# Kernel optimization log

Hardware: AMD Instinct MI355X
Metric: run time of the kernel (lower is better)

The kernel has to match this reference:

```python
import jax, jax.numpy as jnp
import numpy as np

EPS = 1e-8  # torch CosineSimilarity default eps

def _normalize(x):
    # torch clamps each norm at eps before dividing
    n = jnp.sqrt(jnp.sum(x * x, axis=-1, keepdims=True))
    return x / jnp.maximum(n, EPS)

def _cross_entropy(logits, labels):
    logp = jax.nn.log_softmax(logits, axis=-1)
    return -jnp.mean(jnp.take_along_axis(logp, labels[:, None], axis=-1))

def setup_inputs() -> dict:
    key = jax.random.key(0)
    ks = jax.random.split(key, 7)
    B, M, D = 8192, 3129, 512
    return {
        'mm_proj': jax.random.normal(ks[0], (B, D), jnp.float32),
        'ans_embedding': jax.random.normal(ks[1], (M, D), jnp.float32),
        'v_max': jax.random.normal(ks[2], (B, D), jnp.float32),
        'mm': jax.random.normal(ks[3], (B, D), jnp.float32),
        'logits_q': jax.random.normal(ks[4], (B, M), jnp.float32),
        'logits_rubi': jax.random.normal(ks[5], (B, M), jnp.float32),
        'class_id': jax.random.randint(ks[6], (B, 1), 0, M, jnp.int64),
    }

def reference(mm_proj, ans_embedding, v_max, mm, logits_q, logits_rubi, class_id,
              question_loss_weight=1.0):
    cid = class_id.squeeze(1)  # [B]
    # NCE over cosine similarities: fuse normalize + GEMM instead of [B,M,D] expand
    g = _normalize(mm_proj)          # [B, D]
    a = _normalize(ans_embedding)    # [M, D]
    d_logit = jnp.einsum('bd,md->bm', g, a)  # [B, M] cosine matrix
    positive_dist = jnp.take_along_axis(d_logit, cid[:, None], axis=1)[:, 0]  # [B]
    num = jnp.exp(positive_dist)
    den = jnp.sum(jnp.exp(d_logit), axis=-1)
    loss_nce = jnp.mean(-jnp.log(num / den))
    # object cosine loss
    obj_dist = jnp.sum(_normalize(v_max) * _normalize(mm), axis=-1)  # [B]
    obj_loss = jnp.mean(1.0 - obj_dist)
    fusion_loss = (_cross_entropy(logits_rubi, cid) + obj_loss + loss_nce) / 3.0
    question_loss = _cross_entropy(logits_q, cid)
    loss = fusion_loss + question_loss_weight * question_loss
    # out['loss'], out['loss_mm_q'], out['loss_q']
    return jnp.stack([loss, fusion_loss, question_loss])
```

## Files before the change

### kernel.cpp

```cpp
#include <hip/hip_runtime.h>
#include <hip/hip_bf16.h>

#define B_N 8192
#define M_N 3129
#define M_PAD 3200
#define D_N 512

#define CE_L 12
#define CE_SPAN (CE_L * 256)
#define CE_WPA 8344
#define CE_WTOT (2 * CE_WPA)
#define CE1_SPANS 10688
#define CE2_SPANS (CE_WTOT - CE1_SPANS)
#define CE1_BLOCKS (CE1_SPANS / 4)
#define CE2_BLOCKS (CE2_SPANS / 4)

#define PREP_G_BLOCKS   (B_N / 4)
#define PREP_A_BLOCKS   (M_PAD / 4)
#define PREP_OBJ_BLOCKS (B_N / 4)
#define PREP_BLOCKS (PREP_G_BLOCKS + PREP_A_BLOCKS + PREP_OBJ_BLOCKS)

#define GEMM_BLOCKS ((M_PAD / 128) * (B_N / 128))
#define POS_BLOCKS  (B_N / 4)

#define L1_BLOCKS (CE1_BLOCKS + PREP_BLOCKS)
#define L2_BLOCKS (GEMM_BLOCKS + CE2_BLOCKS + POS_BLOCKS)

#define GLOBAL_AS __attribute__((address_space(1)))
#define LDS_AS __attribute__((address_space(3)))

typedef __bf16 bf16x8 __attribute__((ext_vector_type(8)));
typedef float f32x4 __attribute__((ext_vector_type(4)));

__device__ __forceinline__ void ce_span(
    int gw, const float* __restrict__ lq, const float* __restrict__ lr,
    float* __restrict__ rowsum) {
  const int lane = threadIdx.x & 63;
  const int aidx = (gw >= CE_WPA) ? 1 : 0;
  const unsigned wl = (unsigned)(gw - aidx * CE_WPA);
  const unsigned f0 = wl * (unsigned)CE_SPAN;
  const unsigned r0 = f0 / (unsigned)M_N;
  const unsigned b1 = (r0 + 1u) * (unsigned)M_N;
  const float* base = aidx ? lr : lq;
  const float* p = base + f0 + (unsigned)lane * 4u;

  float4 buf[6];
#pragma unroll
  for (int i = 0; i < 6; ++i) buf[i] = *(const float4*)(p + i * 256);

  float a0 = 0.f, a1 = 0.f;
  const unsigned fbase = f0 + (unsigned)lane * 4u;
#pragma unroll
  for (int i = 0; i < CE_L; ++i) {
    float4 v = buf[i % 6];
    if (i + 6 < CE_L) buf[i % 6] = *(const float4*)(p + (i + 6) * 256);
    unsigned f = fbase + (unsigned)i * 256u;
    float e0 = __expf(v.x), e1 = __expf(v.y), e2 = __expf(v.z), e3 = __expf(v.w);
    float lo = 0.f, hi = 0.f;
    if (f + 0u < b1) lo += e0; else hi += e0;
    if (f + 1u < b1) lo += e1; else hi += e1;
    if (f + 2u < b1) lo += e2; else hi += e2;
    if (f + 3u < b1) lo += e3; else hi += e3;
    a0 += lo; a1 += hi;
  }
  for (int o = 1; o < 64; o <<= 1) {
    a0 += __shfl_xor(a0, o);
    a1 += __shfl_xor(a1, o);
  }
  if (lane == 0) {
    float* rs = rowsum + (aidx ? B_N : 0);
    atomicAdd(rs + r0, a0);
    if (a1 != 0.f) atomicAdd(rs + r0 + 1, a1);
  }
}

__device__ __forceinline__ void normalize_row(
    const float* __restrict__ x, __bf16* __restrict__ y,
    int row, int nrows_src, int lane) {
  bf16x8 out;
  if (row >= nrows_src) {
    for (int j = 0; j < 8; ++j) out[j] = (__bf16)0.0f;
    *(bf16x8*)(y + (size_t)row * D_N + lane * 8) = out;
    return;
  }
  const float4* xr = (const float4*)(x + (size_t)row * D_N);
  float4 v0 = xr[lane * 2], v1 = xr[lane * 2 + 1];
  float s = v0.x*v0.x + v0.y*v0.y + v0.z*v0.z + v0.w*v0.w
          + v1.x*v1.x + v1.y*v1.y + v1.z*v1.z + v1.w*v1.w;
  for (int o = 1; o < 64; o <<= 1) s += __shfl_xor(s, o);
  float rn = 1.0f / fmaxf(sqrtf(s), 1e-8f);
  float vals[8] = {v0.x, v0.y, v0.z, v0.w, v1.x, v1.y, v1.z, v1.w};
  for (int j = 0; j < 8; ++j) out[j] = (__bf16)(vals[j] * rn);
  *(bf16x8*)(y + (size_t)row * D_N + lane * 8) = out;
}

__global__ __launch_bounds__(256) void l1_prep_ce_kernel(
    const float* __restrict__ mm_proj, const float* __restrict__ ans_emb,
    const float* __restrict__ v_max, const float* __restrict__ mm,
    const float* __restrict__ lq, const float* __restrict__ lr,
    __bf16* __restrict__ g, __bf16* __restrict__ a,
    float* __restrict__ obj, float* __restrict__ rowsum) {
  int blk = blockIdx.x;
  int wid = threadIdx.x >> 6, lane = threadIdx.x & 63;
  if (blk < CE1_BLOCKS) {
    ce_span(blk * 4 + wid, lq, lr, rowsum);
    return;
  }
  blk -= CE1_BLOCKS;
  if (blk < PREP_G_BLOCKS) {
    normalize_row(mm_proj, g, blk * 4 + wid, B_N, lane);
  } else if (blk < PREP_G_BLOCKS + PREP_A_BLOCKS) {
    normalize_row(ans_emb, a, (blk - PREP_G_BLOCKS) * 4 + wid, M_N, lane);
  } else {
    int b = (blk - PREP_G_BLOCKS - PREP_A_BLOCKS) * 4 + wid;
    const float4* vr = (const float4*)(v_max + (size_t)b * D_N);
    const float4* mr = (const float4*)(mm + (size_t)b * D_N);
    float4 a0 = vr[lane * 2], a1 = vr[lane * 2 + 1];
    float4 b0 = mr[lane * 2], b1 = mr[lane * 2 + 1];
    float sv = a0.x*a0.x + a0.y*a0.y + a0.z*a0.z + a0.w*a0.w
             + a1.x*a1.x + a1.y*a1.y + a1.z*a1.z + a1.w*a1.w;
    float sm = b0.x*b0.x + b0.y*b0.y + b0.z*b0.z + b0.w*b0.w
             + b1.x*b1.x + b1.y*b1.y + b1.z*b1.z + b1.w*b1.w;
    float sd = a0.x*b0.x + a0.y*b0.y + a0.z*b0.z + a0.w*b0.w
             + a1.x*b1.x + a1.y*b1.y + a1.z*b1.z + a1.w*b1.w;
    for (int o = 1; o < 64; o <<= 1) {
      sv += __shfl_xor(sv, o);
      sm += __shfl_xor(sm, o);
      sd += __shfl_xor(sd, o);
    }
    if (lane == 0) {
      float dist = sd / (fmaxf(sqrtf(sv), 1e-8f) * fmaxf(sqrtf(sm), 1e-8f));
      obj[b] = 1.0f - dist;
    }
  }
}

__global__ __launch_bounds__(256) void l2_gemm_ce_pos_kernel(
    const __bf16* __restrict__ g, const __bf16* __restrict__ a,
    const int* __restrict__ cid,
    const float* __restrict__ mm_proj, const float* __restrict__ ans_emb,
    const float* __restrict__ lq, const float* __restrict__ lr,
    float* __restrict__ den, float* __restrict__ pos,
    float* __restrict__ rowsum) {
  __shared__ __bf16 As[128 * 32];
  __shared__ __bf16 Bs[128 * 32];
  int blk = blockIdx.x;
  const int t = threadIdx.x;
  const int lane = t & 63;
  const int wid = t >> 6;

  if (blk < GEMM_BLOCKS) {
    const int brow0 = (blk / (M_PAD / 128)) * 128;
    const int mrow0 = (blk % (M_PAD / 128)) * 128;
    const int wrow = wid >> 1;
    const int wcol = wid & 1;
    const int r = lane & 15;
    const int quad = lane >> 4;

    f32x4 acc[4][4];
    for (int i = 0; i < 4; ++i)
      for (int j = 0; j < 4; ++j)
        acc[i][j] = f32x4{0.f, 0.f, 0.f, 0.f};

    for (int k0 = 0; k0 < D_N; k0 += 32) {
      __syncthreads();
      for (int i = 0; i < 2; ++i) {
        int s = t + i * 256;
        int row = s >> 2;
        int kq = (s & 3) << 3;
        const __bf16* ga = g + (size_t)(brow0 + row) * D_N + (k0 + kq);
        __builtin_amdgcn_global_load_lds((const GLOBAL_AS void*)ga,
                                         (LDS_AS void*)(As + s * 8), 16, 0, 0);
        const __bf16* gb = a + (size_t)(mrow0 + row) * D_N + (k0 + kq);
        __builtin_amdgcn_global_load_lds((const GLOBAL_AS void*)gb,
                                         (LDS_AS void*)(Bs + s * 8), 16, 0, 0);
      }
      __syncthreads();
      bf16x8 af[4], bf[4];
      for (int i = 0; i < 4; ++i)
        af[i] = *(const bf16x8*)(As + (wrow * 64 + i * 16 + r) * 32 + quad * 8);
      for (int j = 0; j < 4; ++j)
        bf[j] = *(const bf16x8*)(Bs + (wcol * 64 + j * 16 + r) * 32 + quad * 8);
      for (int i = 0; i < 4; ++i)
        for (int j = 0; j < 4; ++j)
          acc[i][j] = __builtin_amdgcn_mfma_f32_16x16x32_bf16(af[i], bf[j],
                                                              acc[i][j], 0, 0, 0);
    }

    for (int i = 0; i < 4; ++i) {
      for (int reg = 0; reg < 4; ++reg) {
        float s = 0.0f;
        for (int j = 0; j < 4; ++j) {
          int m = mrow0 + wcol * 64 + j * 16 + r;
          if (m < M_N) s += __expf(acc[i][j][reg]);
        }
        s += __shfl_xor(s, 1);
        s += __shfl_xor(s, 2);
        s += __shfl_xor(s, 4);
        s += __shfl_xor(s, 8);
        if (r == 0) {
          int b = brow0 + wrow * 64 + i * 16 + quad * 4 + reg;
          atomicAdd(den + b, s);
        }
      }
    }
    return;
  }
  blk -= GEMM_BLOCKS;

  if (blk < CE2_BLOCKS) {
    ce_span(CE1_SPANS + blk * 4 + wid, lq, lr, rowsum);
    return;
  }
  blk -= CE2_BLOCKS;

  {
    int b = blk * 4 + wid;
    int label = cid[b];
    const float4* xr = (const float4*)(mm_proj + (size_t)b * D_N);
    float4 v0 = xr[lane * 2], v1 = xr[lane * 2 + 1];
    const float4* yr = (const float4*)(ans_emb + (size_t)label * D_N);
    float4 w0 = yr[lane * 2], w1 = yr[lane * 2 + 1];
    float sg = v0.x*v0.x + v0.y*v0.y + v0.z*v0.z + v0.w*v0.w
             + v1.x*v1.x + v1.y*v1.y + v1.z*v1.z + v1.w*v1.w;
    float sa = w0.x*w0.x + w0.y*w0.y + w0.z*w0.z + w0.w*w0.w
             + w1.x*w1.x + w1.y*w1.y + w1.z*w1.z + w1.w*w1.w;
    for (int o = 1; o < 64; o <<= 1) {
      sg += __shfl_xor(sg, o);
      sa += __shfl_xor(sa, o);
    }
    float rng = 1.0f / fmaxf(sqrtf(sg), 1e-8f);
    float rna = 1.0f / fmaxf(sqrtf(sa), 1e-8f);
    float gv[8] = {v0.x, v0.y, v0.z, v0.w, v1.x, v1.y, v1.z, v1.w};
    float av[8] = {w0.x, w0.y, w0.z, w0.w, w1.x, w1.y, w1.z, w1.w};
    float d = 0.0f;
    for (int j = 0; j < 8; ++j)
      d += (float)(__bf16)(gv[j] * rng) * (float)(__bf16)(av[j] * rna);
    for (int o = 1; o < 64; o <<= 1) d += __shfl_xor(d, o);
    if (lane == 0) pos[b] = d;
  }
}

__global__ __launch_bounds__(256) void final_reduce_kernel(
    const float* __restrict__ den, const float* __restrict__ pos,
    const float* __restrict__ rowsum,
    const float* __restrict__ lq, const float* __restrict__ lr,
    const int* __restrict__ cid, const float* __restrict__ obj,
    float* __restrict__ acc) {
  int b = blockIdx.x * 256 + threadIdx.x;
  int lab = cid[b];
  float xq = lq[(size_t)b * M_N + lab];
  float xr = lr[(size_t)b * M_N + lab];
  float s_nce = logf(den[b]) - pos[b];
  float s_ceq = logf(rowsum[b]) - xq;
  float s_cer = logf(rowsum[B_N + b]) - xr;
  float s_obj = obj[b];
  for (int o = 1; o < 64; o <<= 1) {
    s_nce += __shfl_xor(s_nce, o);
    s_ceq += __shfl_xor(s_ceq, o);
    s_cer += __shfl_xor(s_cer, o);
    s_obj += __shfl_xor(s_obj, o);
  }
  __shared__ float red[4][4];
  int wid = threadIdx.x >> 6;
  if ((threadIdx.x & 63) == 0) {
    red[wid][0] = s_nce; red[wid][1] = s_ceq;
    red[wid][2] = s_cer; red[wid][3] = s_obj;
  }
  __syncthreads();
  if (threadIdx.x < 4) {
    float v = red[0][threadIdx.x] + red[1][threadIdx.x]
            + red[2][threadIdx.x] + red[3][threadIdx.x];
    atomicAdd(acc + threadIdx.x, v);
  }
}

__global__ void final_combine_kernel(const float* __restrict__ acc,
                                     float* __restrict__ out) {
  if (threadIdx.x == 0) {
    float nce = acc[0] / (float)B_N;
    float ceq = acc[1] / (float)B_N;
    float cer = acc[2] / (float)B_N;
    float ob  = acc[3] / (float)B_N;
    float fusion = (cer + ob + nce) * (1.0f / 3.0f);
    out[0] = fusion + ceq;
    out[1] = fusion;
    out[2] = ceq;
  }
}

extern "C" void kernel_launch(void* const* d_in, const int* in_sizes, int n_in,
                              void* d_out, int out_size, void* d_ws, size_t ws_size,
                              hipStream_t stream) {
  const float* mm_proj     = (const float*)d_in[0];
  const float* ans_emb     = (const float*)d_in[1];
  const float* v_max       = (const float*)d_in[2];
  const float* mm          = (const float*)d_in[3];
  const float* logits_q    = (const float*)d_in[4];
  const float* logits_rubi = (const float*)d_in[5];
  const int*   cid         = (const int*)d_in[6];
  float* out = (float*)d_out;

  char* ws = (char*)d_ws;
  __bf16* g = (__bf16*)ws;
  __bf16* a = (__bf16*)(ws + 8388608);
  float* den    = (float*)(ws + 8388608 + 3276800);
  float* rowsum = den + B_N;
  float* acc    = rowsum + 2 * B_N;
  float* pos    = acc + 4;
  float* obj    = pos + B_N;

  hipMemsetAsync(den, 0, (size_t)(3 * B_N + 4) * sizeof(float), stream);

  l1_prep_ce_kernel<<<L1_BLOCKS, 256, 0, stream>>>(
      mm_proj, ans_emb, v_max, mm, logits_q, logits_rubi, g, a, obj, rowsum);
  l2_gemm_ce_pos_kernel<<<L2_BLOCKS, 256, 0, stream>>>(
      g, a, cid, mm_proj, ans_emb, logits_q, logits_rubi, den, pos, rowsum);
  final_reduce_kernel<<<B_N / 256, 256, 0, stream>>>(den, pos, rowsum,
                                                     logits_q, logits_rubi,
                                                     cid, obj, acc);
  final_combine_kernel<<<1, 64, 0, stream>>>(acc, out);
}
```

Measured before the change: 317.5 us.

## Interleave GEMM tiles with CE work, double-buffer LDS, fold memset and combine kernels

Moves all logits cross-entropy work out of the prep kernel and into the GEMM kernel, interleaving blocks so every fifth block is a GEMM tile and the rest are CE or positive-dot blocks. This is meant to overlap memory-bound streaming with MFMA compute. The GEMM k-loop becomes double-buffered so the next stage loads while the current one computes. The memset is replaced by zeroing blocks in the prep kernel, the final combine is folded into the reduce kernel through a last-block counter, and logits reads use nontemporal loads. The cost is more LDS per block and more scheduling-dependent behaviour.

Result: faster. 296.0 us (-6.8%).

```diff
diff --git a/kernel.cpp b/kernel.cpp
--- a/kernel.cpp
+++ b/kernel.cpp
@@ -10,27 +10,28 @@
 #define CE_SPAN (CE_L * 256)
 #define CE_WPA 8344
 #define CE_WTOT (2 * CE_WPA)
-#define CE1_SPANS 10688
-#define CE2_SPANS (CE_WTOT - CE1_SPANS)
-#define CE1_BLOCKS (CE1_SPANS / 4)
-#define CE2_BLOCKS (CE2_SPANS / 4)
+#define CE_BLOCKS (CE_WTOT / 4)
 
 #define PREP_G_BLOCKS   (B_N / 4)
 #define PREP_A_BLOCKS   (M_PAD / 4)
 #define PREP_OBJ_BLOCKS (B_N / 4)
-#define PREP_BLOCKS (PREP_G_BLOCKS + PREP_A_BLOCKS + PREP_OBJ_BLOCKS)
-
-#define GEMM_BLOCKS ((M_PAD / 128) * (B_N / 128))
-#define POS_BLOCKS  (B_N / 4)
-
-#define L1_BLOCKS (CE1_BLOCKS + PREP_BLOCKS)
-#define L2_BLOCKS (GEMM_BLOCKS + CE2_BLOCKS + POS_BLOCKS)
+#define ZERO_FLOATS (3 * B_N + 8)
+#define ZERO_BLOCKS 25
+#define A_BLOCKS (PREP_G_BLOCKS + PREP_A_BLOCKS + PREP_OBJ_BLOCKS + ZERO_BLOCKS)
+
+#define GEMM_TILES ((M_PAD / 128) * (B_N / 128))
+#define B_BLOCKS 8000
+#define POS_BLOCKS_B (B_BLOCKS - GEMM_TILES - CE_BLOCKS)
 
 #define GLOBAL_AS __attribute__((address_space(1)))
 #define LDS_AS __attribute__((address_space(3)))
 
 typedef __bf16 bf16x8 __attribute__((ext_vector_type(8)));
 typedef float f32x4 __attribute__((ext_vector_type(4)));
+
+__device__ __forceinline__ f32x4 nt_load4(const float* p) {
+  return __builtin_nontemporal_load((const f32x4*)p);
+}
 
 __device__ __forceinline__ void ce_span(
     int gw, const float* __restrict__ lq, const float* __restrict__ lr,
@@ -44,16 +45,16 @@
   const float* base = aidx ? lr : lq;
   const float* p = base + f0 + (unsigned)lane * 4u;
 
-  float4 buf[6];
-#pragma unroll
-  for (int i = 0; i < 6; ++i) buf[i] = *(const float4*)(p + i * 256);
+  f32x4 buf[6];
+#pragma unroll
+  for (int i = 0; i < 6; ++i) buf[i] = nt_load4(p + i * 256);
 
   float a0 = 0.f, a1 = 0.f;
   const unsigned fbase = f0 + (unsigned)lane * 4u;
 #pragma unroll
   for (int i = 0; i < CE_L; ++i) {
-    float4 v = buf[i % 6];
-    if (i + 6 < CE_L) buf[i % 6] = *(const float4*)(p + (i + 6) * 256);
+    f32x4 v = buf[i % 6];
+    if (i + 6 < CE_L) buf[i % 6] = nt_load4(p + (i + 6) * 256);
     unsigned f = fbase + (unsigned)i * 256u;
     float e0 = __expf(v.x), e1 = __expf(v.y), e2 = __expf(v.z), e3 = __expf(v.w);
     float lo = 0.f, hi = 0.f;
@@ -83,8 +84,9 @@
     *(bf16x8*)(y + (size_t)row * D_N + lane * 8) = out;
     return;
   }
-  const float4* xr = (const float4*)(x + (size_t)row * D_N);
-  float4 v0 = xr[lane * 2], v1 = xr[lane * 2 + 1];
+  const float* xr = x + (size_t)row * D_N + lane * 8;
+  f32x4 v0 = *(const f32x4*)xr;
+  f32x4 v1 = *(const f32x4*)(xr + 4);
   float s = v0.x*v0.x + v0.y*v0.y + v0.z*v0.z + v0.w*v0.w
           + v1.x*v1.x + v1.y*v1.y + v1.z*v1.z + v1.w*v1.w;
   for (int o = 1; o < 64; o <<= 1) s += __shfl_xor(s, o);
@@ -94,29 +96,23 @@
   *(bf16x8*)(y + (size_t)row * D_N + lane * 8) = out;
 }
 
-__global__ __launch_bounds__(256) void l1_prep_ce_kernel(
+__global__ __launch_bounds__(256) void a_prep_kernel(
     const float* __restrict__ mm_proj, const float* __restrict__ ans_emb,
     const float* __restrict__ v_max, const float* __restrict__ mm,
-    const float* __restrict__ lq, const float* __restrict__ lr,
     __bf16* __restrict__ g, __bf16* __restrict__ a,
-    float* __restrict__ obj, float* __restrict__ rowsum) {
+    float* __restrict__ obj, float* __restrict__ zbase) {
   int blk = blockIdx.x;
   int wid = threadIdx.x >> 6, lane = threadIdx.x & 63;
-  if (blk < CE1_BLOCKS) {
-    ce_span(blk * 4 + wid, lq, lr, rowsum);
-    return;
-  }
-  blk -= CE1_BLOCKS;
   if (blk < PREP_G_BLOCKS) {
     normalize_row(mm_proj, g, blk * 4 + wid, B_N, lane);
   } else if (blk < PREP_G_BLOCKS + PREP_A_BLOCKS) {
     normalize_row(ans_emb, a, (blk - PREP_G_BLOCKS) * 4 + wid, M_N, lane);
-  } else {
+  } else if (blk < PREP_G_BLOCKS + PREP_A_BLOCKS + PREP_OBJ_BLOCKS) {
     int b = (blk - PREP_G_BLOCKS - PREP_A_BLOCKS) * 4 + wid;
-    const float4* vr = (const float4*)(v_max + (size_t)b * D_N);
-    const float4* mr = (const float4*)(mm + (size_t)b * D_N);
-    float4 a0 = vr[lane * 2], a1 = vr[lane * 2 + 1];
-    float4 b0 = mr[lane * 2], b1 = mr[lane * 2 + 1];
+    const float* vr = v_max + (size_t)b * D_N + lane * 8;
+    const float* mr = mm + (size_t)b * D_N + lane * 8;
+    f32x4 a0 = nt_load4(vr), a1 = nt_load4(vr + 4);
+    f32x4 b0 = nt_load4(mr), b1 = nt_load4(mr + 4);
     float sv = a0.x*a0.x + a0.y*a0.y + a0.z*a0.z + a0.w*a0.w
              + a1.x*a1.x + a1.y*a1.y + a1.z*a1.z + a1.w*a1.w;
     float sm = b0.x*b0.x + b0.y*b0.y + b0.z*b0.z + b0.w*b0.w
@@ -132,26 +128,51 @@
       float dist = sd / (fmaxf(sqrtf(sv), 1e-8f) * fmaxf(sqrtf(sm), 1e-8f));
       obj[b] = 1.0f - dist;
     }
-  }
-}
-
-__global__ __launch_bounds__(256) void l2_gemm_ce_pos_kernel(
+  } else {
+    int zb = blk - (PREP_G_BLOCKS + PREP_A_BLOCKS + PREP_OBJ_BLOCKS);
+    int idx = (zb * 256 + threadIdx.x) * 4;
+    if (idx < ZERO_FLOATS) *(f32x4*)(zbase + idx) = f32x4{0.f, 0.f, 0.f, 0.f};
+  }
+}
+
+__device__ __forceinline__ void gemm_stage(
+    const __bf16* __restrict__ g, const __bf16* __restrict__ a,
+    __bf16* As, __bf16* Bs, int t, int brow0, int mrow0, int k0) {
+#pragma unroll
+  for (int i = 0; i < 2; ++i) {
+    int s = t + i * 256;
+    int row = s >> 2;
+    int kq = (s & 3) << 3;
+    const __bf16* ga = g + (size_t)(brow0 + row) * D_N + (k0 + kq);
+    __builtin_amdgcn_global_load_lds((const GLOBAL_AS void*)ga,
+                                     (LDS_AS void*)(As + s * 8), 16, 0, 0);
+    const __bf16* gb = a + (size_t)(mrow0 + row) * D_N + (k0 + kq);
+    __builtin_amdgcn_global_load_lds((const GLOBAL_AS void*)gb,
+                                     (LDS_AS void*)(Bs + s * 8), 16, 0, 0);
+  }
+}
+
+__global__ __launch_bounds__(256) void b_fused_kernel(
     const __bf16* __restrict__ g, const __bf16* __restrict__ a,
     const int* __restrict__ cid,
     const float* __restrict__ mm_proj, const float* __restrict__ ans_emb,
     const float* __restrict__ lq, const float* __restrict__ lr,
     float* __restrict__ den, float* __restrict__ pos,
     float* __restrict__ rowsum) {
-  __shared__ __bf16 As[128 * 32];
-  __shared__ __bf16 Bs[128 * 32];
-  int blk = blockIdx.x;
+  __shared__ __bf16 As[2][128 * 32];
+  __shared__ __bf16 Bs[2][128 * 32];
   const int t = threadIdx.x;
   const int lane = t & 63;
   const int wid = t >> 6;
 
-  if (blk < GEMM_BLOCKS) {
-    const int brow0 = (blk / (M_PAD / 128)) * 128;
-    const int mrow0 = (blk % (M_PAD / 128)) * 128;
+  const int blk = blockIdx.x;
+  const int mod = blk % 5;
+  const int div5 = blk / 5;
+
+  if (mod == 2) {
+    const int tile = div5;
+    const int brow0 = (tile / (M_PAD / 128)) * 128;
+    const int mrow0 = (tile % (M_PAD / 128)) * 128;
     const int wrow = wid >> 1;
     const int wcol = wid & 1;
     const int r = lane & 15;
@@ -162,29 +183,29 @@
       for (int j = 0; j < 4; ++j)
         acc[i][j] = f32x4{0.f, 0.f, 0.f, 0.f};
 
-    for (int k0 = 0; k0 < D_N; k0 += 32) {
+    gemm_stage(g, a, &As[0][0], &Bs[0][0], t, brow0, mrow0, 0);
+    int cur = 0;
+    __syncthreads();
+
+    for (int ks = 0; ks < D_N / 32; ++ks) {
+      if (ks + 1 < D_N / 32)
+        gemm_stage(g, a, &As[cur ^ 1][0], &Bs[cur ^ 1][0], t, brow0, mrow0,
+                   (ks + 1) * 32);
+      bf16x8 af[4], bfr[4];
+#pragma unroll
+      for (int i = 0; i < 4; ++i)
+        af[i] = *(const bf16x8*)(&As[cur][(wrow * 64 + i * 16 + r) * 32 + quad * 8]);
+#pragma unroll
+      for (int j = 0; j < 4; ++j)
+        bfr[j] = *(const bf16x8*)(&Bs[cur][(wcol * 64 + j * 16 + r) * 32 + quad * 8]);
+#pragma unroll
+      for (int i = 0; i < 4; ++i)
+#pragma unroll
+        for (int j = 0; j < 4; ++j)
+          acc[i][j] = __builtin_amdgcn_mfma_f32_16x16x32_bf16(af[i], bfr[j],
+                                                              acc[i][j], 0, 0, 0);
       __syncthreads();
-      for (int i = 0; i < 2; ++i) {
-        int s = t + i * 256;
-        int row = s >> 2;
-        int kq = (s & 3) << 3;
-        const __bf16* ga = g + (size_t)(brow0 + row) * D_N + (k0 + kq);
-        __builtin_amdgcn_global_load_lds((const GLOBAL_AS void*)ga,
-                                         (LDS_AS void*)(As + s * 8), 16, 0, 0);
-        const __bf16* gb = a + (size_t)(mrow0 + row) * D_N + (k0 + kq);
-        __builtin_amdgcn_global_load_lds((const GLOBAL_AS void*)gb,
-                                         (LDS_AS void*)(Bs + s * 8), 16, 0, 0);
-      }
-      __syncthreads();
-      bf16x8 af[4], bf[4];
-      for (int i = 0; i < 4; ++i)
-        af[i] = *(const bf16x8*)(As + (wrow * 64 + i * 16 + r) * 32 + quad * 8);
-      for (int j = 0; j < 4; ++j)
-        bf[j] = *(const bf16x8*)(Bs + (wcol * 64 + j * 16 + r) * 32 + quad * 8);
-      for (int i = 0; i < 4; ++i)
-        for (int j = 0; j < 4; ++j)
-          acc[i][j] = __builtin_amdgcn_mfma_f32_16x16x32_bf16(af[i], bf[j],
-                                                              acc[i][j], 0, 0, 0);
+      cur ^= 1;
     }
 
     for (int i = 0; i < 4; ++i) {
@@ -206,21 +227,21 @@
     }
     return;
   }
-  blk -= GEMM_BLOCKS;
-
-  if (blk < CE2_BLOCKS) {
-    ce_span(CE1_SPANS + blk * 4 + wid, lq, lr, rowsum);
+
+  const int other = div5 * 4 + mod - (mod > 2 ? 1 : 0);
+  if (other < CE_BLOCKS) {
+    ce_span(other * 4 + wid, lq, lr, rowsum);
     return;
   }
-  blk -= CE2_BLOCKS;
 
   {
-    int b = blk * 4 + wid;
+    int b = (other - CE_BLOCKS) * 4 + wid;
+    if (b >= B_N) return;
     int label = cid[b];
-    const float4* xr = (const float4*)(mm_proj + (size_t)b * D_N);
-    float4 v0 = xr[lane * 2], v1 = xr[lane * 2 + 1];
-    const float4* yr = (const float4*)(ans_emb + (size_t)label * D_N);
-    float4 w0 = yr[lane * 2], w1 = yr[lane * 2 + 1];
+    const float* xr = mm_proj + (size_t)b * D_N + lane * 8;
+    f32x4 v0 = *(const f32x4*)xr, v1 = *(const f32x4*)(xr + 4);
+    const float* yr = ans_emb + (size_t)label * D_N + lane * 8;
+    f32x4 w0 = *(const f32x4*)yr, w1 = *(const f32x4*)(yr + 4);
     float sg = v0.x*v0.x + v0.y*v0.y + v0.z*v0.z + v0.w*v0.w
              + v1.x*v1.x + v1.y*v1.y + v1.z*v1.z + v1.w*v1.w;
     float sa = w0.x*w0.x + w0.y*w0.y + w0.z*w0.z + w0.w*w0.w
@@ -241,12 +262,12 @@
   }
 }
 
-__global__ __launch_bounds__(256) void final_reduce_kernel(
+__global__ __launch_bounds__(256) void c_final_kernel(
     const float* __restrict__ den, const float* __restrict__ pos,
     const float* __restrict__ rowsum,
     const float* __restrict__ lq, const float* __restrict__ lr,
     const int* __restrict__ cid, const float* __restrict__ obj,
-    float* __restrict__ acc) {
+    float* __restrict__ acc, float* __restrict__ out) {
   int b = blockIdx.x * 256 + threadIdx.x;
   int lab = cid[b];
   float xq = lq[(size_t)b * M_N + lab];
@@ -273,19 +294,19 @@
             + red[2][threadIdx.x] + red[3][threadIdx.x];
     atomicAdd(acc + threadIdx.x, v);
   }
-}
-
-__global__ void final_combine_kernel(const float* __restrict__ acc,
-                                     float* __restrict__ out) {
   if (threadIdx.x == 0) {
-    float nce = acc[0] / (float)B_N;
-    float ceq = acc[1] / (float)B_N;
-    float cer = acc[2] / (float)B_N;
-    float ob  = acc[3] / (float)B_N;
-    float fusion = (cer + ob + nce) * (1.0f / 3.0f);
-    out[0] = fusion + ceq;
-    out[1] = fusion;
-    out[2] = ceq;
+    __threadfence();
+    unsigned prev = atomicAdd((unsigned*)(acc + 4), 1u);
+    if (prev == 31u) {
+      float nce = atomicAdd(acc + 0, 0.0f) / (float)B_N;
+      float ceq = atomicAdd(acc + 1, 0.0f) / (float)B_N;
+      float cer = atomicAdd(acc + 2, 0.0f) / (float)B_N;
+      float ob  = atomicAdd(acc + 3, 0.0f) / (float)B_N;
+      float fusion = (cer + ob + nce) * (1.0f / 3.0f);
+      out[0] = fusion + ceq;
+      out[1] = fusion;
+      out[2] = ceq;
+    }
   }
 }
 
@@ -307,17 +328,13 @@
   float* den    = (float*)(ws + 8388608 + 3276800);
   float* rowsum = den + B_N;
   float* acc    = rowsum + 2 * B_N;
-  float* pos    = acc + 4;
+  float* pos    = acc + 8;
   float* obj    = pos + B_N;
 
-  hipMemsetAsync(den, 0, (size_t)(3 * B_N + 4) * sizeof(float), stream);
-
-  l1_prep_ce_kernel<<<L1_BLOCKS, 256, 0, stream>>>(
-      mm_proj, ans_emb, v_max, mm, logits_q, logits_rubi, g, a, obj, rowsum);
-  l2_gemm_ce_pos_kernel<<<L2_BLOCKS, 256, 0, stream>>>(
+  a_prep_kernel<<<A_BLOCKS, 256, 0, stream>>>(
+      mm_proj, ans_emb, v_max, mm, g, a, obj, den);
+  b_fused_kernel<<<B_BLOCKS, 256, 0, stream>>>(
       g, a, cid, mm_proj, ans_emb, logits_q, logits_rubi, den, pos, rowsum);
-  final_reduce_kernel<<<B_N / 256, 256, 0, stream>>>(den, pos, rowsum,
-                                                     logits_q, logits_rubi,
-                                                     cid, obj, acc);
-  final_combine_kernel<<<1, 64, 0, stream>>>(acc, out);
-}
+  c_final_kernel<<<B_N / 256, 256, 0, stream>>>(
+      den, pos, rowsum, logits_q, logits_rubi, cid, obj, acc, out);
+}
```
